# Performance work log

Hardware: AMD Instinct MI355X
Metric: run time of the kernel (lower is better)

The kernel has to match this reference:

```python
import jax, jax.numpy as jnp
import numpy as np

H = 2048
M = 256
B, S = 8, 4096


def setup_inputs() -> dict:
    key = jax.random.key(0)
    k1, k2, k3, k4 = jax.random.split(key, 4)
    x = jax.random.normal(k1, (B, S, H), dtype=jnp.float32)
    memory = jax.random.normal(k2, (M, H), dtype=jnp.float32)
    w_write = jax.random.normal(k3, (H, H), dtype=jnp.float32) / np.sqrt(H)
    b_write = jax.random.normal(k4, (H,), dtype=jnp.float32) * 0.01
    return {"x": x, "memory": memory, "w_write": w_write, "b_write": b_write}


def reference(x, memory, w_write, b_write):
    # Read path: tiny cross-attention against fixed memory slots.
    # scores: [B, S, M]
    read_weights = jax.nn.softmax(jnp.einsum('bsh,mh->bsm', x, memory), axis=-1)
    read_memory = jnp.einsum('bsm,mh->bsh', read_weights, memory)  # [B, S, H]

    # Write path: mean-pool over sequence, linear, EMA update of memory.
    write_content = x.mean(axis=1) @ w_write.T + b_write  # [B, H]
    # Faithful to the torch code: broadcast [M,H] with [B,1,H] -> [B,M,H]
    new_memory = 0.9 * memory[None, :, :] + 0.1 * write_content[:, None, :]

    combined = jnp.concatenate([x, read_memory], axis=-1)  # [B, S, 2H]
    return (combined, read_memory, new_memory)
```

## Files before the change

kernel.cpp:

```cpp
#include <hip/hip_runtime.h>


#define H_DIM 2048
#define M_SLOT 256
#define N_B 8
#define N_S 4096
#define N_ROWS 32768
#define TM 64
#define BK 32
#define N_CHUNK 64

typedef __bf16 bf16x8 __attribute__((ext_vector_type(8)));
typedef float floatx4 __attribute__((ext_vector_type(4)));

#define WS_MEMQ_HI ((size_t)0)
#define WS_MEMQ_LO ((size_t)1 << 20)
#define WS_MEMT2   ((size_t)2 << 20)
#define WS_WQ      ((size_t)3 << 20)
#define WS_XSUM    ((size_t)20 << 20)
#define WS_WC      ((size_t)21 << 20)

#define OUT_COMBINED ((size_t)0)
#define OUT_READMEM  ((size_t)134217728)
#define OUT_NEWMEM   ((size_t)201326592)

#define L_AHI 0
#define L_ALO 4096
#define L_BHI 8192
#define L_BLO 24576
#define L_COLSUM 40960
#define L_SMAX 49152
#define L_SSUM 50176
#define L_GMAX 51200
#define L_GINV 51456
#define L_TOTAL 51712

__device__ __forceinline__ floatx4 mfma16(bf16x8 a, bf16x8 b, floatx4 c) {
  return __builtin_amdgcn_mfma_f32_16x16x32_bf16(a, b, c, 0, 0, 0);
}

__global__ __launch_bounds__(256) void prep_kernel(const float* __restrict__ mem,
                                                   unsigned char* __restrict__ ws) {
  const int t = threadIdx.x;
  const int blk = blockIdx.x;
  if (blk < 256) {
    const int idx = blk * 256 + t;
    const int q = idx >> 8, n = idx & 255;
    const float* src = mem + (size_t)n * H_DIM + q * 8;
    bf16x8 hv, lv;
#pragma unroll
    for (int j = 0; j < 8; j++) {
      float v = src[j];
      __bf16 hh = (__bf16)v;
      hv[j] = hh;
      lv[j] = (__bf16)(v - (float)hh);
    }
    *(bf16x8*)(ws + WS_MEMQ_HI + (size_t)idx * 16) = hv;
    *(bf16x8*)(ws + WS_MEMQ_LO + (size_t)idx * 16) = lv;
  } else {
    const int idx = (blk - 256) * 256 + t;
    const int sq = idx >> 11, h = idx & 2047;
    bf16x8 v;
#pragma unroll
    for (int j = 0; j < 8; j++)
      v[j] = (__bf16)mem[(size_t)(sq * 8 + j) * H_DIM + h];
    *(bf16x8*)(ws + WS_MEMT2 + (size_t)idx * 16) = v;
  }
}

__global__ __launch_bounds__(256, 2) void gemm1_softmax(
    const float* __restrict__ x, unsigned char* __restrict__ ws,
    float* __restrict__ out) {
  __shared__ __align__(16) unsigned char smem[L_TOTAL];
  const int t = threadIdx.x;
  const int blk = blockIdx.x;
  const int row0 = blk * TM;
  const int bidx = blk >> 6;
  const int wv = t >> 6, lane = t & 63, r = lane & 15, qd = lane >> 4;

  float* colsum = (float*)(smem + L_COLSUM);
  for (int i = t; i < H_DIM; i += 256) colsum[i] = 0.0f;

  floatx4 acc[4][4];
#pragma unroll
  for (int a = 0; a < 4; a++)
#pragma unroll
    for (int b = 0; b < 4; b++) {
      floatx4 z = {0.f, 0.f, 0.f, 0.f};
      acc[a][b] = z;
    }

  const int xr = t >> 2, kq = t & 3;
  for (int c = 0; c < N_CHUNK; c++) {
    __syncthreads();
    const float* xp = x + (size_t)(row0 + xr) * H_DIM + c * BK + kq * 8;
    float4 v0 = *(const float4*)xp;
    float4 v1 = *(const float4*)(xp + 4);
    float* cp = out + OUT_COMBINED + (size_t)(row0 + xr) * 4096 + c * BK + kq * 8;
    *(float4*)cp = v0;
    *(float4*)(cp + 4) = v1;
    float vv[8] = {v0.x, v0.y, v0.z, v0.w, v1.x, v1.y, v1.z, v1.w};
#pragma unroll
    for (int j = 0; j < 8; j++) atomicAdd(&colsum[c * BK + kq * 8 + j], vv[j]);
    bf16x8 hv, lv;
#pragma unroll
    for (int j = 0; j < 8; j++) {
      __bf16 hh = (__bf16)vv[j];
      hv[j] = hh;
      lv[j] = (__bf16)(vv[j] - (float)hh);
    }
    *(bf16x8*)(smem + L_AHI + kq * 1024 + xr * 16) = hv;
    *(bf16x8*)(smem + L_ALO + kq * 1024 + xr * 16) = lv;
    const unsigned char* gh = ws + WS_MEMQ_HI + (size_t)c * 16384;
    const unsigned char* gl = ws + WS_MEMQ_LO + (size_t)c * 16384;
#pragma unroll
    for (int i = 0; i < 4; i++) {
      int p = i * 256 + t;
      *(uint4*)(smem + L_BHI + p * 16) = *(const uint4*)(gh + (size_t)p * 16);
      *(uint4*)(smem + L_BLO + p * 16) = *(const uint4*)(gl + (size_t)p * 16);
    }
    __syncthreads();
    bf16x8 ah[4], al[4], bh[4], bl[4];
#pragma unroll
    for (int rt = 0; rt < 4; rt++) {
      ah[rt] = *(const bf16x8*)(smem + L_AHI + qd * 1024 + (rt * 16 + r) * 16);
      al[rt] = *(const bf16x8*)(smem + L_ALO + qd * 1024 + (rt * 16 + r) * 16);
    }
#pragma unroll
    for (int ct = 0; ct < 4; ct++) {
      int n = wv * 64 + ct * 16 + r;
      bh[ct] = *(const bf16x8*)(smem + L_BHI + qd * 4096 + n * 16);
      bl[ct] = *(const bf16x8*)(smem + L_BLO + qd * 4096 + n * 16);
    }
#pragma unroll
    for (int rt = 0; rt < 4; rt++)
#pragma unroll
      for (int ct = 0; ct < 4; ct++) {
        acc[rt][ct] = mfma16(ah[rt], bh[ct], acc[rt][ct]);
        acc[rt][ct] = mfma16(ah[rt], bl[ct], acc[rt][ct]);
        acc[rt][ct] = mfma16(al[rt], bh[ct], acc[rt][ct]);
      }
  }
  {
    float* xsum = (float*)(ws + WS_XSUM);
    for (int i = t; i < H_DIM; i += 256)
      atomicAdd(&xsum[bidx * H_DIM + i], colsum[i]);
  }
  float* smax = (float*)(smem + L_SMAX);
  float* ssum = (float*)(smem + L_SSUM);
  float* gmax = (float*)(smem + L_GMAX);
  float* ginv = (float*)(smem + L_GINV);
#pragma unroll
  for (int rt = 0; rt < 4; rt++)
#pragma unroll
    for (int rg = 0; rg < 4; rg++) {
      float m = fmaxf(fmaxf(acc[rt][0][rg], acc[rt][1][rg]),
                      fmaxf(acc[rt][2][rg], acc[rt][3][rg]));
#pragma unroll
      for (int off = 1; off < 16; off <<= 1) m = fmaxf(m, __shfl_xor(m, off));
      if (r == 0) smax[wv * 64 + rt * 16 + qd * 4 + rg] = m;
    }
  __syncthreads();
  if (t < 64)
    gmax[t] = fmaxf(fmaxf(smax[t], smax[64 + t]),
                    fmaxf(smax[128 + t], smax[192 + t]));
  __syncthreads();
#pragma unroll
  for (int rt = 0; rt < 4; rt++)
#pragma unroll
    for (int rg = 0; rg < 4; rg++) {
      const int row = rt * 16 + qd * 4 + rg;
      const float gm = gmax[row];
      float s = 0.f;
#pragma unroll
      for (int ct = 0; ct < 4; ct++) {
        float e = __expf(acc[rt][ct][rg] - gm);
        acc[rt][ct][rg] = e;
        s += e;
      }
#pragma unroll
      for (int off = 1; off < 16; off <<= 1) s += __shfl_xor(s, off);
      if (r == 0) ssum[wv * 64 + row] = s;
    }
  __syncthreads();
  if (t < 64)
    ginv[t] = 1.0f / (ssum[t] + ssum[64 + t] + ssum[128 + t] + ssum[192 + t]);
  __syncthreads();
  __bf16* wl = (__bf16*)smem;
#pragma unroll
  for (int rt = 0; rt < 4; rt++)
#pragma unroll
    for (int rg = 0; rg < 4; rg++) {
      const int row = rt * 16 + qd * 4 + rg;
      const float gi = ginv[row];
#pragma unroll
      for (int ct = 0; ct < 4; ct++) {
        const int col = wv * 64 + ct * 16 + r;
        wl[row * 264 + col] = (__bf16)(acc[rt][ct][rg] * gi);
      }
    }
  __syncthreads();
  unsigned char* wq = ws + WS_WQ + (size_t)blk * 32768;
#pragma unroll
  for (int i = 0; i < 8; i++) {
    const int p = i * 256 + t;
    const int q = p >> 6, rowl = p & 63;
    *(uint4*)(wq + (size_t)p * 16) =
        *(const uint4*)(smem + ((size_t)rowl * 264 + q * 8) * 2);
  }
}

__global__ __launch_bounds__(256, 2) void gemm2_kernel(
    const unsigned char* __restrict__ ws, float* __restrict__ out) {
  __shared__ __align__(16) unsigned char smem[49152];
  const int t = threadIdx.x;
  const int rtb = blockIdx.x >> 3, hc = blockIdx.x & 7;
  const int row0 = rtb * 64, h0 = hc * 256;
  const int wv = t >> 6, lane = t & 63, r = lane & 15, qd = lane >> 4;

  const unsigned char* wq = ws + WS_WQ + (size_t)rtb * 32768;
#pragma unroll
  for (int i = 0; i < 8; i++) {
    const int p = i * 256 + t;
    *(uint4*)(smem + p * 16) = *(const uint4*)(wq + (size_t)p * 16);
  }
  floatx4 acc[4][4];
#pragma unroll
  for (int a = 0; a < 4; a++)
#pragma unroll
    for (int b = 0; b < 4; b++) {
      floatx4 z = {0.f, 0.f, 0.f, 0.f};
      acc[a][b] = z;
    }
  for (int ks = 0; ks < 8; ks++) {
    __syncthreads();
#pragma unroll
    for (int i = 0; i < 4; i++) {
      const int p = i * 256 + t;
      const int sql = p >> 8, hh = p & 255;
      *(uint4*)(smem + 32768 + p * 16) =
          *(const uint4*)(ws + WS_MEMT2 +
                          ((size_t)(ks * 4 + sql) * 2048 + h0 + hh) * 16);
    }
    __syncthreads();
    bf16x8 a[4], b[4];
#pragma unroll
    for (int rt = 0; rt < 4; rt++)
      a[rt] = *(const bf16x8*)(smem + (ks * 4 + qd) * 1024 + (rt * 16 + r) * 16);
#pragma unroll
    for (int ct = 0; ct < 4; ct++)
      b[ct] = *(const bf16x8*)(smem + 32768 + qd * 4096 +
                               (wv * 64 + ct * 16 + r) * 16);
#pragma unroll
    for (int rt = 0; rt < 4; rt++)
#pragma unroll
      for (int ct = 0; ct < 4; ct++)
        acc[rt][ct] = mfma16(a[rt], b[ct], acc[rt][ct]);
  }
#pragma unroll
  for (int rt = 0; rt < 4; rt++)
#pragma unroll
    for (int ct = 0; ct < 4; ct++)
#pragma unroll
      for (int rg = 0; rg < 4; rg++) {
        const int R = row0 + rt * 16 + qd * 4 + rg;
        const int hcol = h0 + wv * 64 + ct * 16 + r;
        const float v = acc[rt][ct][rg];
        out[OUT_READMEM + (size_t)R * 2048 + hcol] = v;
        out[OUT_COMBINED + (size_t)R * 4096 + 2048 + hcol] = v;
      }
}

__global__ __launch_bounds__(256) void write_gemm(
    const float* __restrict__ w_write, const float* __restrict__ b_write,
    unsigned char* __restrict__ ws) {
  const int t = threadIdx.x;
  const int j = blockIdx.x * 64 + (t >> 2);
  const int pr = t & 3;
  const float* xsum = (const float*)(ws + WS_XSUM);
  const float* wr = w_write + (size_t)j * H_DIM;
  const float* x0p = xsum + pr * H_DIM;
  const float* x1p = xsum + (pr + 4) * H_DIM;
  float a0 = 0.f, a1 = 0.f;
  for (int h = 0; h < H_DIM; h += 4) {
    float4 w4 = *(const float4*)(wr + h);
    float4 x0 = *(const float4*)(x0p + h);
    float4 x1 = *(const float4*)(x1p + h);
    a0 += w4.x * x0.x + w4.y * x0.y + w4.z * x0.z + w4.w * x0.w;
    a1 += w4.x * x1.x + w4.y * x1.y + w4.z * x1.z + w4.w * x1.w;
  }
  float* wc = (float*)(ws + WS_WC);
  const float bw = b_write[j];
  wc[pr * H_DIM + j] = a0 * (1.f / 4096.f) + bw;
  wc[(pr + 4) * H_DIM + j] = a1 * (1.f / 4096.f) + bw;
}

__global__ __launch_bounds__(256) void newmem_kernel(
    const float* __restrict__ mem, const unsigned char* __restrict__ ws,
    float* __restrict__ out) {
  const int i4 = blockIdx.x * 256 + threadIdx.x;
  const size_t e = (size_t)i4 * 4;
  const int b = (int)(e >> 19);
  const int rem = (int)(e & 524287);
  const int h = (int)(e & 2047);
  const float4 mv = *(const float4*)(mem + rem);
  const float* wc = (const float*)(ws + WS_WC);
  const float4 wv = *(const float4*)(wc + b * H_DIM + h);
  float4 o;
  o.x = 0.9f * mv.x + 0.1f * wv.x;
  o.y = 0.9f * mv.y + 0.1f * wv.y;
  o.z = 0.9f * mv.z + 0.1f * wv.z;
  o.w = 0.9f * mv.w + 0.1f * wv.w;
  *(float4*)(out + OUT_NEWMEM + e) = o;
}

extern "C" void kernel_launch(void* const* d_in, const int* in_sizes, int n_in,
                              void* d_out, int out_size, void* d_ws, size_t ws_size,
                              hipStream_t stream) {
  const float* x = (const float*)d_in[0];
  const float* memory = (const float*)d_in[1];
  const float* w_write = (const float*)d_in[2];
  const float* b_write = (const float*)d_in[3];
  float* out = (float*)d_out;
  unsigned char* ws = (unsigned char*)d_ws;

  prep_kernel<<<512, 256, 0, stream>>>(memory, ws);
  hipMemsetAsync(ws + WS_XSUM, 0, (size_t)N_B * H_DIM * sizeof(float), stream);
  gemm1_softmax<<<512, 256, 0, stream>>>(x, ws, out);
  gemm2_kernel<<<4096, 256, 0, stream>>>(ws, out);
  write_gemm<<<32, 256, 0, stream>>>(w_write, b_write, ws);
  newmem_kernel<<<4096, 256, 0, stream>>>(memory, ws, out);
}
```

Measured before the change: 1.508 ms.

## Async LDS loads, double-buffer gemm2, remap blocks, and widen write_gemm parallelism

Memory-slot tiles in gemm1 and gemm2 are now loaded straight into LDS with global_load_lds, and gemm2 double-buffers its B tile so the next k-slice loads while the current one is multiplied. In gemm1 the x chunk is prefetched into registers one iteration ahead. Block indices in both GEMMs are remapped so that neighbouring workgroups touch different row groups, which changes cache and channel locality. write_gemm is split over 256 blocks, each thread covering a quarter of K, and partial sums are combined with shuffles, raising parallelism in that small kernel. gemm2 now uses 64KB of LDS, which may limit occupancy, and the async-copy synchronization relies on __syncthreads ordering.

```diff
diff --git a/kernel.cpp b/kernel.cpp
--- a/kernel.cpp
+++ b/kernel.cpp
@@ -35,8 +35,19 @@
 #define L_GINV 51456
 #define L_TOTAL 51712
 
+#define G2_A 0
+#define G2_B0 32768
+#define G2_B1 49152
+#define G2_TOTAL 65536
+
 __device__ __forceinline__ floatx4 mfma16(bf16x8 a, bf16x8 b, floatx4 c) {
   return __builtin_amdgcn_mfma_f32_16x16x32_bf16(a, b, c, 0, 0, 0);
+}
+
+__device__ __forceinline__ void async16(const void* g, void* l) {
+  __builtin_amdgcn_global_load_lds(
+      (const __attribute__((address_space(1))) void*)g,
+      (__attribute__((address_space(3))) void*)l, 16, 0, 0);
 }
 
 __global__ __launch_bounds__(256) void prep_kernel(const float* __restrict__ mem,
@@ -73,7 +84,8 @@
     float* __restrict__ out) {
   __shared__ __align__(16) unsigned char smem[L_TOTAL];
   const int t = threadIdx.x;
-  const int blk = blockIdx.x;
+  const int orig = blockIdx.x;
+  const int blk = (orig & 7) * 64 + (orig >> 3);
   const int row0 = blk * TM;
   const int bidx = blk >> 6;
   const int wv = t >> 6, lane = t & 63, r = lane & 15, qd = lane >> 4;
@@ -91,14 +103,26 @@
     }
 
   const int xr = t >> 2, kq = t & 3;
+  const float* xbase = x + (size_t)(row0 + xr) * H_DIM + kq * 8;
+  float* cbase = out + OUT_COMBINED + (size_t)(row0 + xr) * 4096 + kq * 8;
+
+  float4 v0 = *(const float4*)(xbase);
+  float4 v1 = *(const float4*)(xbase + 4);
+
   for (int c = 0; c < N_CHUNK; c++) {
     __syncthreads();
-    const float* xp = x + (size_t)(row0 + xr) * H_DIM + c * BK + kq * 8;
-    float4 v0 = *(const float4*)xp;
-    float4 v1 = *(const float4*)(xp + 4);
-    float* cp = out + OUT_COMBINED + (size_t)(row0 + xr) * 4096 + c * BK + kq * 8;
-    *(float4*)cp = v0;
-    *(float4*)(cp + 4) = v1;
+    {
+      const unsigned char* gh = ws + WS_MEMQ_HI + (size_t)c * 16384;
+      const unsigned char* gl = ws + WS_MEMQ_LO + (size_t)c * 16384;
+#pragma unroll
+      for (int i = 0; i < 4; i++) {
+        const int p = i * 256 + t;
+        async16(gh + (size_t)p * 16, smem + L_BHI + p * 16);
+        async16(gl + (size_t)p * 16, smem + L_BLO + p * 16);
+      }
+    }
+    *(float4*)(cbase + c * BK) = v0;
+    *(float4*)(cbase + c * BK + 4) = v1;
     float vv[8] = {v0.x, v0.y, v0.z, v0.w, v1.x, v1.y, v1.z, v1.w};
 #pragma unroll
     for (int j = 0; j < 8; j++) atomicAdd(&colsum[c * BK + kq * 8 + j], vv[j]);
@@ -111,15 +135,11 @@
     }
     *(bf16x8*)(smem + L_AHI + kq * 1024 + xr * 16) = hv;
     *(bf16x8*)(smem + L_ALO + kq * 1024 + xr * 16) = lv;
-    const unsigned char* gh = ws + WS_MEMQ_HI + (size_t)c * 16384;
-    const unsigned char* gl = ws + WS_MEMQ_LO + (size_t)c * 16384;
-#pragma unroll
-    for (int i = 0; i < 4; i++) {
-      int p = i * 256 + t;
-      *(uint4*)(smem + L_BHI + p * 16) = *(const uint4*)(gh + (size_t)p * 16);
-      *(uint4*)(smem + L_BLO + p * 16) = *(const uint4*)(gl + (size_t)p * 16);
-    }
     __syncthreads();
+    if (c + 1 < N_CHUNK) {
+      v0 = *(const float4*)(xbase + (size_t)(c + 1) * BK);
+      v1 = *(const float4*)(xbase + (size_t)(c + 1) * BK + 4);
+    }
     bf16x8 ah[4], al[4], bh[4], bl[4];
 #pragma unroll
     for (int rt = 0; rt < 4; rt++) {
@@ -212,9 +232,11 @@
 
 __global__ __launch_bounds__(256, 2) void gemm2_kernel(
     const unsigned char* __restrict__ ws, float* __restrict__ out) {
-  __shared__ __align__(16) unsigned char smem[49152];
+  __shared__ __align__(16) unsigned char smem[G2_TOTAL];
   const int t = threadIdx.x;
-  const int rtb = blockIdx.x >> 3, hc = blockIdx.x & 7;
+  const int orig = blockIdx.x;
+  const int lb = (orig & 7) * 512 + (orig >> 3);
+  const int rtb = lb >> 3, hc = lb & 7;
   const int row0 = rtb * 64, h0 = hc * 256;
   const int wv = t >> 6, lane = t & 63, r = lane & 15, qd = lane >> 4;
 
@@ -222,7 +244,14 @@
 #pragma unroll
   for (int i = 0; i < 8; i++) {
     const int p = i * 256 + t;
-    *(uint4*)(smem + p * 16) = *(const uint4*)(wq + (size_t)p * 16);
+    async16(wq + (size_t)p * 16, smem + G2_A + p * 16);
+  }
+#pragma unroll
+  for (int i = 0; i < 4; i++) {
+    const int p = i * 256 + t;
+    const int sql = p >> 8, hh = p & 255;
+    async16(ws + WS_MEMT2 + ((size_t)sql * 2048 + h0 + hh) * 16,
+            smem + G2_B0 + p * 16);
   }
   floatx4 acc[4][4];
 #pragma unroll
@@ -232,30 +261,36 @@
       floatx4 z = {0.f, 0.f, 0.f, 0.f};
       acc[a][b] = z;
     }
+  __syncthreads();
+
   for (int ks = 0; ks < 8; ks++) {
-    __syncthreads();
-#pragma unroll
-    for (int i = 0; i < 4; i++) {
-      const int p = i * 256 + t;
-      const int sql = p >> 8, hh = p & 255;
-      *(uint4*)(smem + 32768 + p * 16) =
-          *(const uint4*)(ws + WS_MEMT2 +
-                          ((size_t)(ks * 4 + sql) * 2048 + h0 + hh) * 16);
-    }
-    __syncthreads();
+    const int boff = (ks & 1) ? G2_B1 : G2_B0;
+    const int noff = (ks & 1) ? G2_B0 : G2_B1;
+    if (ks + 1 < 8) {
+#pragma unroll
+      for (int i = 0; i < 4; i++) {
+        const int p = i * 256 + t;
+        const int sql = p >> 8, hh = p & 255;
+        async16(ws + WS_MEMT2 +
+                    ((size_t)((ks + 1) * 4 + sql) * 2048 + h0 + hh) * 16,
+                smem + noff + p * 16);
+      }
+    }
     bf16x8 a[4], b[4];
 #pragma unroll
     for (int rt = 0; rt < 4; rt++)
-      a[rt] = *(const bf16x8*)(smem + (ks * 4 + qd) * 1024 + (rt * 16 + r) * 16);
+      a[rt] = *(const bf16x8*)(smem + G2_A + (ks * 4 + qd) * 1024 +
+                               (rt * 16 + r) * 16);
 #pragma unroll
     for (int ct = 0; ct < 4; ct++)
-      b[ct] = *(const bf16x8*)(smem + 32768 + qd * 4096 +
+      b[ct] = *(const bf16x8*)(smem + boff + qd * 4096 +
                                (wv * 64 + ct * 16 + r) * 16);
 #pragma unroll
     for (int rt = 0; rt < 4; rt++)
 #pragma unroll
       for (int ct = 0; ct < 4; ct++)
         acc[rt][ct] = mfma16(a[rt], b[ct], acc[rt][ct]);
+    __syncthreads();
   }
 #pragma unroll
   for (int rt = 0; rt < 4; rt++)
@@ -275,24 +310,25 @@
     const float* __restrict__ w_write, const float* __restrict__ b_write,
     unsigned char* __restrict__ ws) {
   const int t = threadIdx.x;
-  const int j = blockIdx.x * 64 + (t >> 2);
-  const int pr = t & 3;
+  const int j = blockIdx.x * 8 + (t >> 5);
+  const int pr = t & 31;
+  const int b = pr & 7;
+  const int kq = pr >> 3;
   const float* xsum = (const float*)(ws + WS_XSUM);
-  const float* wr = w_write + (size_t)j * H_DIM;
-  const float* x0p = xsum + pr * H_DIM;
-  const float* x1p = xsum + (pr + 4) * H_DIM;
-  float a0 = 0.f, a1 = 0.f;
-  for (int h = 0; h < H_DIM; h += 4) {
+  const float* wr = w_write + (size_t)j * H_DIM + kq * 512;
+  const float* xp = xsum + (size_t)b * H_DIM + kq * 512;
+  float a0 = 0.f;
+  for (int h = 0; h < 512; h += 4) {
     float4 w4 = *(const float4*)(wr + h);
-    float4 x0 = *(const float4*)(x0p + h);
-    float4 x1 = *(const float4*)(x1p + h);
+    float4 x0 = *(const float4*)(xp + h);
     a0 += w4.x * x0.x + w4.y * x0.y + w4.z * x0.z + w4.w * x0.w;
-    a1 += w4.x * x1.x + w4.y * x1.y + w4.z * x1.z + w4.w * x1.w;
-  }
-  float* wc = (float*)(ws + WS_WC);
-  const float bw = b_write[j];
-  wc[pr * H_DIM + j] = a0 * (1.f / 4096.f) + bw;
-  wc[(pr + 4) * H_DIM + j] = a1 * (1.f / 4096.f) + bw;
+  }
+  a0 += __shfl_xor(a0, 8);
+  a0 += __shfl_xor(a0, 16);
+  if (kq == 0) {
+    float* wc = (float*)(ws + WS_WC);
+    wc[(size_t)b * H_DIM + j] = a0 * (1.0f / 4096.f) + b_write[j];
+  }
 }
 
 __global__ __launch_bounds__(256) void newmem_kernel(
@@ -328,6 +364,6 @@
   hipMemsetAsync(ws + WS_XSUM, 0, (size_t)N_B * H_DIM * sizeof(float), stream);
   gemm1_softmax<<<512, 256, 0, stream>>>(x, ws, out);
   gemm2_kernel<<<4096, 256, 0, stream>>>(ws, out);
-  write_gemm<<<32, 256, 0, stream>>>(w_write, b_write, ws);
+  write_gemm<<<256, 256, 0, stream>>>(w_write, b_write, ws);
   newmem_kernel<<<4096, 256, 0, stream>>>(memory, ws, out);
 }
```

Result: faster. 1.393 ms (-7.6%).
